# Optimization experiments

Hardware: AMD Instinct MI355X
Metric: run time of the kernel (lower is better)

## Reference

```python
import jax, jax.numpy as jnp
import numpy as np

HOURS = 24
ALPHA, BETA, GAMMA, DELTA = 1.0, 2.0, 1.0, 0.5
TEMP = 0.1
WIN = 2  # window_size in _peak_shape_loss
NEG = -1e9

B, S = 16384, 1440  # 60 days of hourly data


def setup_inputs() -> dict:
    key = jax.random.key(0)
    k1, k2 = jax.random.split(key)
    y_pred = jax.random.normal(k1, (B, S), dtype=jnp.float32)
    y_true = jax.random.normal(k2, (B, S), dtype=jnp.float32)
    # default daytime mask from the module: hour in [6, 20]
    hours = jnp.tile(jnp.arange(HOURS), S // HOURS)  # (S,)
    day = ((hours >= 6) & (hours <= 20)).astype(jnp.float32)
    is_daytime = jnp.broadcast_to(day, (B, S))
    return {"y_pred": y_pred, "y_true": y_true, "is_daytime": is_daytime}


def _soft_peaks(y, day_mask):
    # y, day_mask: (B, D, H) -> soft peak values/times per day: (B, D)
    masked = jnp.where(day_mask > 0.5, y, NEG)
    attn = jax.nn.softmax(masked / TEMP, axis=-1)
    vals = jnp.sum(attn * y, axis=-1)
    t = jnp.arange(HOURS, dtype=y.dtype)
    times = jnp.sum(attn * t, axis=-1)
    return vals, times


def reference(y_pred, y_true, is_daytime):
    b, s = y_true.shape
    d = s // HOURS
    yp = y_pred[:, : d * HOURS].reshape(b, d, HOURS)
    yt = y_true[:, : d * HOURS].reshape(b, d, HOURS)
    dm = is_daytime[:, : d * HOURS].reshape(b, d, HOURS)

    L_overall = jnp.mean((y_pred - y_true) ** 2)

    tv, tt = _soft_peaks(yt, dm)
    pv, pt = _soft_peaks(yp, dm)
    L_mag = jnp.mean((pv - tv) ** 2)
    L_time = jnp.mean((pt - tt) ** 2)

    masked_true = jnp.where(dm > 0.5, yt, NEG)
    peak = jnp.argmax(masked_true, axis=-1)  # (B, D) int
    offs = jnp.arange(-WIN, WIN + 1)
    idx = peak[..., None] + offs  # (B, D, 5)
    valid = (idx >= 0) & (idx < HOURS)  # emulates window clipping at day edges
    idx_c = jnp.clip(idx, 0, HOURS - 1)
    tw = jnp.take_along_axis(yt, idx_c, axis=-1)  # (B, D, 5)
    pw = jnp.take_along_axis(yp, idx_c, axis=-1)
    vmask = valid.astype(yt.dtype)
    cnt = jnp.sum(vmask, axis=-1)  # window length per (B, D)
    tmax = jnp.max(jnp.where(valid, tw, -jnp.inf), axis=-1, keepdims=True)
    pmax = jnp.max(jnp.where(valid, pw, -jnp.inf), axis=-1, keepdims=True)
    tn = tw / (tmax + 1e-6)
    pn = pw / (pmax + 1e-6)
    per = jnp.sum((pn - tn) ** 2 * vmask, axis=-1) / cnt  # per-window MSE
    L_shape = jnp.sum(per) / (b * d + 1e-6)

    return ALPHA * L_overall + BETA * L_mag + GAMMA * L_time + DELTA * L_shape
```

## Files before the change

### kernel.cpp

```cpp
#include <hip/hip_runtime.h>
#include <math.h>


#define HOURS_ 24
#define WIN_ 2
#define NEGV (-1e9f)

__global__ __launch_bounds__(256) void splloss_days(
    const float* __restrict__ ypred,
    const float* __restrict__ ytrue,
    const float* __restrict__ isday,
    float4* __restrict__ partials,
    int n_days)
{
    const int tid  = threadIdx.x;
    const int half = tid & 1;
    const int h0g  = half * 12;
    const int dayStride = (gridDim.x * 256) >> 1;

    float o = 0.f, mg = 0.f, tl = 0.f, sh = 0.f;

    for (int day = (blockIdx.x * 256 + tid) >> 1; day < n_days; day += dayStride) {
        const float4* p4 = reinterpret_cast<const float4*>(ypred + (size_t)day * 24 + h0g);
        const float4* t4 = reinterpret_cast<const float4*>(ytrue + (size_t)day * 24 + h0g);
        const float4* d4 = reinterpret_cast<const float4*>(isday + (size_t)day * 24 + h0g);
        float4 pa0 = p4[0], pa1 = p4[1], pa2 = p4[2];
        float4 ta0 = t4[0], ta1 = t4[1], ta2 = t4[2];
        float4 da0 = d4[0], da1 = d4[1], da2 = d4[2];

        float a[12] = {pa0.x, pa0.y, pa0.z, pa0.w, pa1.x, pa1.y, pa1.z, pa1.w,
                       pa2.x, pa2.y, pa2.z, pa2.w};
        float b[12] = {ta0.x, ta0.y, ta0.z, ta0.w, ta1.x, ta1.y, ta1.z, ta1.w,
                       ta2.x, ta2.y, ta2.z, ta2.w};
        float dm[12] = {da0.x, da0.y, da0.z, da0.w, da1.x, da1.y, da1.z, da1.w,
                        da2.x, da2.y, da2.z, da2.w};

        #pragma unroll
        for (int k = 0; k < 12; ++k) { float d = a[k] - b[k]; o += d * d; }

        float mt = -INFINITY, mp = -INFINITY;
        int pk = h0g;
        #pragma unroll
        for (int k = 0; k < 12; ++k) {
            bool dy = dm[k] > 0.5f;
            float bm = dy ? b[k] : NEGV;
            float am = dy ? a[k] : NEGV;
            if (bm > mt) { mt = bm; pk = h0g + k; }
            mp = fmaxf(mp, am);
        }
        {
            float mt_o = __shfl_xor(mt, 1);
            int   pk_o = __shfl_xor(pk, 1);
            float mp_o = __shfl_xor(mp, 1);
            bool takeo = (mt_o > mt) || (mt_o == mt && pk_o < pk);
            pk = takeo ? pk_o : pk;
            mt = fmaxf(mt, mt_o);
            mp = fmaxf(mp, mp_o);
        }

        float set = 0.f, syt = 0.f, sht = 0.f;
        float sep = 0.f, syp = 0.f, shp = 0.f;
        #pragma unroll
        for (int k = 0; k < 12; ++k) {
            bool dy = dm[k] > 0.5f;
            float bm = dy ? b[k] : NEGV;
            float am = dy ? a[k] : NEGV;
            float et = __expf((bm - mt) * 10.f);
            float ep = __expf((am - mp) * 10.f);
            float hh = (float)(h0g + k);
            set += et; syt += et * b[k]; sht += et * hh;
            sep += ep; syp += ep * a[k]; shp += ep * hh;
        }
        set += __shfl_xor(set, 1);
        syt += __shfl_xor(syt, 1);
        sht += __shfl_xor(sht, 1);
        sep += __shfl_xor(sep, 1);
        syp += __shfl_xor(syp, 1);
        shp += __shfl_xor(shp, 1);
        {
            float tv = syt / set, tt = sht / set;
            float pv = syp / sep, pt = shp / sep;
            float dmg = (pv - tv) * (pv - tv);
            float dtl = (pt - tt) * (pt - tt);
            mg += half ? 0.f : dmg;
            tl += half ? 0.f : dtl;
        }

        int lo = pk - WIN_; if (lo < 0) lo = 0;
        int hi = pk + WIN_; if (hi > 23) hi = 23;
        float cnt = (float)(hi - lo + 1);
        float twmax = -INFINITY, pwmax = -INFINITY;
        #pragma unroll
        for (int k = 0; k < 12; ++k) {
            int hg = h0g + k;
            bool in = (hg >= lo) && (hg <= hi);
            twmax = in ? fmaxf(twmax, b[k]) : twmax;
            pwmax = in ? fmaxf(pwmax, a[k]) : pwmax;
        }
        twmax = fmaxf(twmax, __shfl_xor(twmax, 1));
        pwmax = fmaxf(pwmax, __shfl_xor(pwmax, 1));
        {
            float rt = 1.f / (twmax + 1e-6f);
            float rp = 1.f / (pwmax + 1e-6f);
            float ss = 0.f;
            #pragma unroll
            for (int k = 0; k < 12; ++k) {
                int hg = h0g + k;
                bool in = (hg >= lo) && (hg <= hi);
                float d = a[k] * rp - b[k] * rt;
                ss += in ? d * d : 0.f;
            }
            sh += ss / cnt;
        }
    }

    #pragma unroll
    for (int off = 32; off > 0; off >>= 1) {
        o  += __shfl_down(o,  off);
        mg += __shfl_down(mg, off);
        tl += __shfl_down(tl, off);
        sh += __shfl_down(sh, off);
    }
    __shared__ float4 red[4];
    int wid = threadIdx.x >> 6;
    if ((threadIdx.x & 63) == 0) red[wid] = make_float4(o, mg, tl, sh);
    __syncthreads();
    if (threadIdx.x == 0) {
        float4 r0 = red[0], r1 = red[1], r2 = red[2], r3 = red[3];
        partials[blockIdx.x] = make_float4(r0.x + r1.x + r2.x + r3.x,
                                           r0.y + r1.y + r2.y + r3.y,
                                           r0.z + r1.z + r2.z + r3.z,
                                           r0.w + r1.w + r2.w + r3.w);
    }
}

__global__ __launch_bounds__(256) void splloss_final(
    const float4* __restrict__ partials, int nb, float* __restrict__ out,
    double inv_bs, double inv_bd, double inv_shape)
{
    double o = 0.0, m = 0.0, t = 0.0, s = 0.0;
    for (int i = threadIdx.x; i < nb; i += 256) {
        float4 p = partials[i];
        o += (double)p.x; m += (double)p.y; t += (double)p.z; s += (double)p.w;
    }
    #pragma unroll
    for (int off = 32; off > 0; off >>= 1) {
        o += __shfl_down(o, off);
        m += __shfl_down(m, off);
        t += __shfl_down(t, off);
        s += __shfl_down(s, off);
    }
    __shared__ double red[4][4];
    int wid = threadIdx.x >> 6;
    if ((threadIdx.x & 63) == 0) { red[wid][0] = o; red[wid][1] = m; red[wid][2] = t; red[wid][3] = s; }
    __syncthreads();
    if (threadIdx.x == 0) {
        double ot = red[0][0] + red[1][0] + red[2][0] + red[3][0];
        double mt = red[0][1] + red[1][1] + red[2][1] + red[3][1];
        double tt = red[0][2] + red[1][2] + red[2][2] + red[3][2];
        double st = red[0][3] + red[1][3] + red[2][3] + red[3][3];
        double total = 1.0 * (ot * inv_bs)
                     + 2.0 * (mt * inv_bd)
                     + 1.0 * (tt * inv_bd)
                     + 0.5 * (st * inv_shape);
        out[0] = (float)total;
    }
}

extern "C" void kernel_launch(void* const* d_in, const int* in_sizes, int n_in,
                              void* d_out, int out_size, void* d_ws, size_t ws_size,
                              hipStream_t stream) {
    const float* yp = (const float*)d_in[0];
    const float* yt = (const float*)d_in[1];
    const float* dm = (const float*)d_in[2];
    float* out = (float*)d_out;

    int n = in_sizes[0];
    int n_days = n / HOURS_;

    int nb = 1920;
    int nbMax = (n_days + 127) / 128;
    if (nbMax < nb) nb = nbMax;

    float4* partials = (float4*)d_ws;

    splloss_days<<<nb, 256, 0, stream>>>(yp, yt, dm, partials, n_days);

    double inv_bs    = 1.0 / (double)n;
    double inv_bd    = 1.0 / (double)n_days;
    double inv_shape = 1.0 / ((double)n_days + 1e-6);
    splloss_final<<<1, 256, 0, stream>>>(partials, nb, out, inv_bs, inv_bd, inv_shape);
}
```

Baseline: 268.3 us.

## Process two days per thread pair with all loads issued upfront

Replaces the grid-stride loop with a fixed launch in which each thread pair handles exactly two days, issuing all eighteen float4 loads before any compute so more memory requests are in flight per thread. The per-day work is pulled into an inlined helper that uses tree-structured argmax/max reductions, fma forms, hardware reciprocal, and a lookup for the window-count reciprocal. The grid size is now derived from the number of days rather than capped at 1920 blocks, which gives more blocks and a larger partials array for the final reduction. The approximate reciprocal may slightly change numerics.

Measured after the change: 268.9 us. Within noise of the previous version (+0.2%).

```diff
diff --git a/kernel.cpp b/kernel.cpp
--- a/kernel.cpp
+++ b/kernel.cpp
@@ -5,6 +5,120 @@
 #define HOURS_ 24
 #define WIN_ 2
 #define NEGV (-1e9f)
+
+__device__ __forceinline__ float frcp(float x) { return __builtin_amdgcn_rcpf(x); }
+
+__device__ __forceinline__ void day_body(
+    float4 pa0, float4 pa1, float4 pa2,
+    float4 ta0, float4 ta1, float4 ta2,
+    float4 da0, float4 da1, float4 da2,
+    int h0g, int half,
+    float& o, float& mg, float& tl, float& sh)
+{
+    float a[12] = {pa0.x, pa0.y, pa0.z, pa0.w, pa1.x, pa1.y, pa1.z, pa1.w,
+                   pa2.x, pa2.y, pa2.z, pa2.w};
+    float b[12] = {ta0.x, ta0.y, ta0.z, ta0.w, ta1.x, ta1.y, ta1.z, ta1.w,
+                   ta2.x, ta2.y, ta2.z, ta2.w};
+    float dv[12] = {da0.x, da0.y, da0.z, da0.w, da1.x, da1.y, da1.z, da1.w,
+                    da2.x, da2.y, da2.z, da2.w};
+    float bm[12], am[12];
+    #pragma unroll
+    for (int k = 0; k < 12; ++k) {
+        bool dy = dv[k] > 0.5f;
+        bm[k] = dy ? b[k] : NEGV;
+        am[k] = dy ? a[k] : NEGV;
+    }
+
+    #pragma unroll
+    for (int k = 0; k < 12; ++k) { float d = a[k] - b[k]; o = fmaf(d, d, o); }
+
+    float tv_[6]; int ti_[6];
+    #pragma unroll
+    for (int k = 0; k < 6; ++k) {
+        bool t = bm[2*k+1] > bm[2*k];
+        tv_[k] = t ? bm[2*k+1] : bm[2*k];
+        ti_[k] = t ? (h0g + 2*k+1) : (h0g + 2*k);
+    }
+    #pragma unroll
+    for (int k = 0; k < 3; ++k) {
+        bool t = tv_[2*k+1] > tv_[2*k];
+        tv_[k] = t ? tv_[2*k+1] : tv_[2*k];
+        ti_[k] = t ? ti_[2*k+1] : ti_[2*k];
+    }
+    bool t01 = tv_[1] > tv_[0];
+    float fv = t01 ? tv_[1] : tv_[0];
+    int   fi = t01 ? ti_[1] : ti_[0];
+    bool t2  = tv_[2] > fv;
+    float mt = t2 ? tv_[2] : fv;
+    int   pk = t2 ? ti_[2] : fi;
+
+    float mpa = fmaxf(fmaxf(am[0], am[1]), am[2]);
+    float mpb = fmaxf(fmaxf(am[3], am[4]), am[5]);
+    float mpc = fmaxf(fmaxf(am[6], am[7]), am[8]);
+    float mpd = fmaxf(fmaxf(am[9], am[10]), am[11]);
+    float mp  = fmaxf(fmaxf(mpa, mpb), fmaxf(mpc, mpd));
+
+    {
+        float mt_o = __shfl_xor(mt, 1);
+        int   pk_o = __shfl_xor(pk, 1);
+        float mp_o = __shfl_xor(mp, 1);
+        bool takeo = (mt_o > mt) || (mt_o == mt && pk_o < pk);
+        pk = takeo ? pk_o : pk;
+        mt = fmaxf(mt, mt_o);
+        mp = fmaxf(mp, mp_o);
+    }
+
+    float mt10 = mt * 10.f, mp10 = mp * 10.f;
+    float set = 0.f, syt = 0.f, sht = 0.f;
+    float sep = 0.f, syp = 0.f, shp = 0.f;
+    #pragma unroll
+    for (int k = 0; k < 12; ++k) {
+        float et = __expf(fmaf(bm[k], 10.f, -mt10));
+        float ep = __expf(fmaf(am[k], 10.f, -mp10));
+        float hh = (float)(h0g + k);
+        set += et; syt = fmaf(et, b[k], syt); sht = fmaf(et, hh, sht);
+        sep += ep; syp = fmaf(ep, a[k], syp); shp = fmaf(ep, hh, shp);
+    }
+    set += __shfl_xor(set, 1); syt += __shfl_xor(syt, 1); sht += __shfl_xor(sht, 1);
+    sep += __shfl_xor(sep, 1); syp += __shfl_xor(syp, 1); shp += __shfl_xor(shp, 1);
+    {
+        float rs = frcp(set), rq = frcp(sep);
+        float tvv = syt * rs, ttv = sht * rs;
+        float pvv = syp * rq, ptv = shp * rq;
+        float d1 = pvv - tvv, d2 = ptv - ttv;
+        float dmg = d1 * d1, dtl = d2 * d2;
+        mg += half ? 0.f : dmg;
+        tl += half ? 0.f : dtl;
+    }
+
+    int lo = pk - WIN_; lo = lo < 0 ? 0 : lo;
+    int hi = pk + WIN_; hi = hi > 23 ? 23 : hi;
+    int cnt = hi - lo + 1;
+    float invcnt = (cnt == 5) ? 0.2f : ((cnt == 4) ? 0.25f : (1.f / 3.f));
+    float twm = -INFINITY, pwm = -INFINITY;
+    #pragma unroll
+    for (int k = 0; k < 12; ++k) {
+        int hg = h0g + k;
+        bool in = (hg >= lo) && (hg <= hi);
+        twm = in ? fmaxf(twm, b[k]) : twm;
+        pwm = in ? fmaxf(pwm, a[k]) : pwm;
+    }
+    twm = fmaxf(twm, __shfl_xor(twm, 1));
+    pwm = fmaxf(pwm, __shfl_xor(pwm, 1));
+    {
+        float rt  = frcp(twm + 1e-6f);
+        float rpw = frcp(pwm + 1e-6f);
+        float ss = 0.f;
+        #pragma unroll
+        for (int k = 0; k < 12; ++k) {
+            int hg = h0g + k;
+            bool in = (hg >= lo) && (hg <= hi);
+            float d = fmaf(a[k], rpw, -(b[k] * rt));
+            ss = in ? fmaf(d, d, ss) : ss;
+        }
+        sh = fmaf(ss, invcnt, sh);
+    }
+}
 
 __global__ __launch_bounds__(256) void splloss_days(
     const float* __restrict__ ypred,
@@ -16,103 +130,38 @@
     const int tid  = threadIdx.x;
     const int half = tid & 1;
     const int h0g  = half * 12;
-    const int dayStride = (gridDim.x * 256) >> 1;
-
-    float o = 0.f, mg = 0.f, tl = 0.f, sh = 0.f;
-
-    for (int day = (blockIdx.x * 256 + tid) >> 1; day < n_days; day += dayStride) {
-        const float4* p4 = reinterpret_cast<const float4*>(ypred + (size_t)day * 24 + h0g);
-        const float4* t4 = reinterpret_cast<const float4*>(ytrue + (size_t)day * 24 + h0g);
-        const float4* d4 = reinterpret_cast<const float4*>(isday + (size_t)day * 24 + h0g);
-        float4 pa0 = p4[0], pa1 = p4[1], pa2 = p4[2];
-        float4 ta0 = t4[0], ta1 = t4[1], ta2 = t4[2];
-        float4 da0 = d4[0], da1 = d4[1], da2 = d4[2];
-
-        float a[12] = {pa0.x, pa0.y, pa0.z, pa0.w, pa1.x, pa1.y, pa1.z, pa1.w,
-                       pa2.x, pa2.y, pa2.z, pa2.w};
-        float b[12] = {ta0.x, ta0.y, ta0.z, ta0.w, ta1.x, ta1.y, ta1.z, ta1.w,
-                       ta2.x, ta2.y, ta2.z, ta2.w};
-        float dm[12] = {da0.x, da0.y, da0.z, da0.w, da1.x, da1.y, da1.z, da1.w,
-                        da2.x, da2.y, da2.z, da2.w};
-
-        #pragma unroll
-        for (int k = 0; k < 12; ++k) { float d = a[k] - b[k]; o += d * d; }
-
-        float mt = -INFINITY, mp = -INFINITY;
-        int pk = h0g;
-        #pragma unroll
-        for (int k = 0; k < 12; ++k) {
-            bool dy = dm[k] > 0.5f;
-            float bm = dy ? b[k] : NEGV;
-            float am = dy ? a[k] : NEGV;
-            if (bm > mt) { mt = bm; pk = h0g + k; }
-            mp = fmaxf(mp, am);
-        }
-        {
-            float mt_o = __shfl_xor(mt, 1);
-            int   pk_o = __shfl_xor(pk, 1);
-            float mp_o = __shfl_xor(mp, 1);
-            bool takeo = (mt_o > mt) || (mt_o == mt && pk_o < pk);
-            pk = takeo ? pk_o : pk;
-            mt = fmaxf(mt, mt_o);
-            mp = fmaxf(mp, mp_o);
-        }
-
-        float set = 0.f, syt = 0.f, sht = 0.f;
-        float sep = 0.f, syp = 0.f, shp = 0.f;
-        #pragma unroll
-        for (int k = 0; k < 12; ++k) {
-            bool dy = dm[k] > 0.5f;
-            float bm = dy ? b[k] : NEGV;
-            float am = dy ? a[k] : NEGV;
-            float et = __expf((bm - mt) * 10.f);
-            float ep = __expf((am - mp) * 10.f);
-            float hh = (float)(h0g + k);
-            set += et; syt += et * b[k]; sht += et * hh;
-            sep += ep; syp += ep * a[k]; shp += ep * hh;
-        }
-        set += __shfl_xor(set, 1);
-        syt += __shfl_xor(syt, 1);
-        sht += __shfl_xor(sht, 1);
-        sep += __shfl_xor(sep, 1);
-        syp += __shfl_xor(syp, 1);
-        shp += __shfl_xor(shp, 1);
-        {
-            float tv = syt / set, tt = sht / set;
-            float pv = syp / sep, pt = shp / sep;
-            float dmg = (pv - tv) * (pv - tv);
-            float dtl = (pt - tt) * (pt - tt);
-            mg += half ? 0.f : dmg;
-            tl += half ? 0.f : dtl;
-        }
-
-        int lo = pk - WIN_; if (lo < 0) lo = 0;
-        int hi = pk + WIN_; if (hi > 23) hi = 23;
-        float cnt = (float)(hi - lo + 1);
-        float twmax = -INFINITY, pwmax = -INFINITY;
-        #pragma unroll
-        for (int k = 0; k < 12; ++k) {
-            int hg = h0g + k;
-            bool in = (hg >= lo) && (hg <= hi);
-            twmax = in ? fmaxf(twmax, b[k]) : twmax;
-            pwmax = in ? fmaxf(pwmax, a[k]) : pwmax;
-        }
-        twmax = fmaxf(twmax, __shfl_xor(twmax, 1));
-        pwmax = fmaxf(pwmax, __shfl_xor(pwmax, 1));
-        {
-            float rt = 1.f / (twmax + 1e-6f);
-            float rp = 1.f / (pwmax + 1e-6f);
-            float ss = 0.f;
-            #pragma unroll
-            for (int k = 0; k < 12; ++k) {
-                int hg = h0g + k;
-                bool in = (hg >= lo) && (hg <= hi);
-                float d = a[k] * rp - b[k] * rt;
-                ss += in ? d * d : 0.f;
-            }
-            sh += ss / cnt;
-        }
-    }
+    const int pair = blockIdx.x * 128 + (tid >> 1);
+    const int strideDays = gridDim.x * 128;
+
+    const int day0 = pair;
+    const int day1 = pair + strideDays;
+    const bool v0 = day0 < n_days;
+    const bool v1 = day1 < n_days;
+    const int d0 = v0 ? day0 : 0;
+    const int d1 = v1 ? day1 : 0;
+
+    const float4* A0 = reinterpret_cast<const float4*>(ypred + (size_t)d0 * 24 + h0g);
+    const float4* B0 = reinterpret_cast<const float4*>(ytrue + (size_t)d0 * 24 + h0g);
+    const float4* D0 = reinterpret_cast<const float4*>(isday + (size_t)d0 * 24 + h0g);
+    const float4* A1 = reinterpret_cast<const float4*>(ypred + (size_t)d1 * 24 + h0g);
+    const float4* B1 = reinterpret_cast<const float4*>(ytrue + (size_t)d1 * 24 + h0g);
+    const float4* D1 = reinterpret_cast<const float4*>(isday + (size_t)d1 * 24 + h0g);
+    float4 pa0 = A0[0], pa1 = A0[1], pa2 = A0[2];
+    float4 ta0 = B0[0], ta1 = B0[1], ta2 = B0[2];
+    float4 da0 = D0[0], da1 = D0[1], da2 = D0[2];
+    float4 qa0 = A1[0], qa1 = A1[1], qa2 = A1[2];
+    float4 ua0 = B1[0], ua1 = B1[1], ua2 = B1[2];
+    float4 ea0 = D1[0], ea1 = D1[1], ea2 = D1[2];
+
+    float o0 = 0.f, mg0 = 0.f, tl0 = 0.f, sh0 = 0.f;
+    float o1 = 0.f, mg1 = 0.f, tl1 = 0.f, sh1 = 0.f;
+    day_body(pa0, pa1, pa2, ta0, ta1, ta2, da0, da1, da2, h0g, half, o0, mg0, tl0, sh0);
+    day_body(qa0, qa1, qa2, ua0, ua1, ua2, ea0, ea1, ea2, h0g, half, o1, mg1, tl1, sh1);
+
+    float o  = (v0 ? o0  : 0.f) + (v1 ? o1  : 0.f);
+    float mg = (v0 ? mg0 : 0.f) + (v1 ? mg1 : 0.f);
+    float tl = (v0 ? tl0 : 0.f) + (v1 ? tl1 : 0.f);
+    float sh = (v0 ? sh0 : 0.f) + (v1 ? sh1 : 0.f);
 
     #pragma unroll
     for (int off = 32; off > 0; off >>= 1) {
@@ -178,9 +227,7 @@
     int n = in_sizes[0];
     int n_days = n / HOURS_;
 
-    int nb = 1920;
-    int nbMax = (n_days + 127) / 128;
-    if (nbMax < nb) nb = nbMax;
+    int nb = (n_days + 255) / 256;
 
     float4* partials = (float4*)d_ws;
 
```
